# Kernel optimization log

Hardware: AMD Instinct MI355X
Metric: run time of the kernel (lower is better)

## Reference

```python
import jax, jax.numpy as jnp
from jax import lax
import numpy as np

NUM_LAYERS = 256
EPS = 1e-12


def setup_inputs() -> dict:
    key = jax.random.key(0)
    # values in [0.9, 1.1) so the 256-step multiplicative chain stays O(1)
    x = 0.9 + 0.2 * jax.random.uniform(key, (4, 19, 512, 512), dtype=jnp.float32)
    return {"x": x}


def _maxpool3x3_same(x):
    # torch MaxPool2d(kernel=3, stride=1, padding=1): pad value acts as -inf
    return lax.reduce_window(
        x, -jnp.inf, lax.max,
        window_dimensions=(1, 1, 3, 3),
        window_strides=(1, 1, 1, 1),
        padding=[(0, 0), (0, 0), (1, 1), (1, 1)],
    )


def reference(x):
    initial = x
    cur = -x
    one = jnp.float32(1.0)
    cur = cur.at[:, :, 0, :].set(one)
    cur = cur.at[:, :, -1, :].set(one)
    cur = cur.at[:, :, :, 0].set(one)
    cur = cur.at[:, :, :, -1].set(one)

    def step(c, _):
        return _maxpool3x3_same(c) * initial, None

    cur, _ = lax.scan(step, cur, None, length=NUM_LAYERS)
    # F.normalize default: L2 over dim=1, eps=1e-12
    norm = jnp.sqrt(jnp.sum(cur * cur, axis=1, keepdims=True))
    normed = cur / jnp.maximum(norm, EPS)
    return normed * initial
```

## Files before the change

### kernel.cpp

```cpp
#include <hip/hip_runtime.h>
#include <math.h>

#define BB 4
#define CC 19
#define HH 512
#define WW 512
#define NSLICE (BB * CC)
#define SLICE  (HH * WW)
#define W4     (WW / 4)
#define EPS    1e-12f
#define NEGINF (-INFINITY)

#define TSTEPS 16
#define RROWS  64
#define AROWS  96
#define NPASS  16
#define RBLK   8

#define TX   64
#define TY   8
#define COLS 8
#define ROWS 12
#define THREADS 512

struct F8 { float4 a, b; };

__device__ __forceinline__ float dpp_up(float src) {
    int o = __builtin_amdgcn_update_dpp(__float_as_int(NEGINF), __float_as_int(src),
                                        0x138 , 0xF, 0xF, false);
    return __int_as_float(o);
}
__device__ __forceinline__ float dpp_dn(float src) {
    int o = __builtin_amdgcn_update_dpp(__float_as_int(NEGINF), __float_as_int(src),
                                        0x130 , 0xF, 0xF, false);
    return __int_as_float(o);
}

__global__ void init_kernel(const float* __restrict__ x, float* __restrict__ cur) {
    int t = blockIdx.x * blockDim.x + threadIdx.x;
    const float4* x4 = (const float4*)x;
    float4* c4 = (float4*)cur;
    float4 v = x4[t];
    int pix = t << 2;
    int s = pix & (SLICE - 1);
    int i = s >> 9;
    int j0 = s & 511;
    float4 o;
    o.x = -v.x; o.y = -v.y; o.z = -v.z; o.w = -v.w;
    if (i == 0 || i == HH - 1) {
        o.x = 1.0f; o.y = 1.0f; o.z = 1.0f; o.w = 1.0f;
    } else {
        if (j0 == 0)        o.x = 1.0f;
        if (j0 == WW - 4)   o.w = 1.0f;
    }
    c4[t] = o;
}

__global__ __launch_bounds__(THREADS, 1)
void pass_kernel(const float* __restrict__ in, const float* __restrict__ xg,
                 float* __restrict__ out) {
    const int tid  = threadIdx.x;
    const int tx   = tid & 63;
    const int ty   = tid >> 6;
    const int g    = (blockIdx.x & 7) * (NSLICE * RBLK / 8) + (blockIdx.x >> 3);
    const int bc   = g / RBLK;
    const int brow = g % RBLK;
    const int gstart = brow * RROWS - TSTEPS;
    const int row0   = gstart + ty * ROWS;
    const int col0   = tx * COLS;
    const size_t sbase = (size_t)bc * SLICE;

    __shared__ float Tb[2][TY][TX * 9];
    __shared__ float Bb[2][TY][TX * 9];

    const float4 neg4 = make_float4(NEGINF, NEGINF, NEGINF, NEGINF);
    const float4 one4 = make_float4(1.f, 1.f, 1.f, 1.f);

    float4 cl[ROWS], cr[ROWS], xl[ROWS], xr_[ROWS];

#pragma unroll
    for (int r = 0; r < ROWS; ++r) {
        int grow = row0 + r;
        if (grow >= 0 && grow < HH) {
            const float4* p = (const float4*)(in + sbase + (size_t)grow * WW + col0);
            cl[r] = p[0]; cr[r] = p[1];
            const float4* q = (const float4*)(xg + sbase + (size_t)grow * WW + col0);
            xl[r] = q[0]; xr_[r] = q[1];
        } else {
            cl[r] = neg4; cr[r] = neg4; xl[r] = one4; xr_[r] = one4;
        }
    }

    auto hrow = [&](float4 a, float4 b) -> F8 {
        float lpx = dpp_up(b.w);
        float rpx = dpp_dn(a.x);
        F8 h;
        h.a.x = fmaxf(fmaxf(lpx, a.x), a.y);
        h.a.y = fmaxf(fmaxf(a.x, a.y), a.z);
        h.a.z = fmaxf(fmaxf(a.y, a.z), a.w);
        h.a.w = fmaxf(fmaxf(a.z, a.w), b.x);
        h.b.x = fmaxf(fmaxf(a.w, b.x), b.y);
        h.b.y = fmaxf(fmaxf(b.x, b.y), b.z);
        h.b.z = fmaxf(fmaxf(b.y, b.z), b.w);
        h.b.w = fmaxf(fmaxf(b.z, b.w), rpx);
        return h;
    };

    for (int t = 0; t < TSTEPS; ++t) {
        const int buf = t & 1;
        float* tp = &Tb[buf][ty][tx * 9];
        float* bp = &Bb[buf][ty][tx * 9];
        tp[0] = cl[0].x;  tp[1] = cl[0].y;  tp[2] = cl[0].z;  tp[3] = cl[0].w;
        tp[4] = cr[0].x;  tp[5] = cr[0].y;  tp[6] = cr[0].z;  tp[7] = cr[0].w;
        bp[0] = cl[11].x; bp[1] = cl[11].y; bp[2] = cl[11].z; bp[3] = cl[11].w;
        bp[4] = cr[11].x; bp[5] = cr[11].y; bp[6] = cr[11].z; bp[7] = cr[11].w;
        __syncthreads();

        float4 upA, upB, dnA, dnB;
        if (ty > 0) {
            const float* q = &Bb[buf][ty - 1][tx * 9];
            upA = make_float4(q[0], q[1], q[2], q[3]);
            upB = make_float4(q[4], q[5], q[6], q[7]);
        } else { upA = neg4; upB = neg4; }
        if (ty < TY - 1) {
            const float* q = &Tb[buf][ty + 1][tx * 9];
            dnA = make_float4(q[0], q[1], q[2], q[3]);
            dnB = make_float4(q[4], q[5], q[6], q[7]);
        } else { dnA = neg4; dnB = neg4; }

        F8 hA = hrow(upA, upB);
        F8 hB = hrow(cl[0], cr[0]);
#pragma unroll
        for (int r = 0; r < ROWS; ++r) {
            F8 hC;
            if (r + 1 < ROWS) hC = hrow(cl[r + 1], cr[r + 1]);
            else              hC = hrow(dnA, dnB);
            float4 vl, vr;
            vl.x = fmaxf(fmaxf(hA.a.x, hB.a.x), hC.a.x);
            vl.y = fmaxf(fmaxf(hA.a.y, hB.a.y), hC.a.y);
            vl.z = fmaxf(fmaxf(hA.a.z, hB.a.z), hC.a.z);
            vl.w = fmaxf(fmaxf(hA.a.w, hB.a.w), hC.a.w);
            vr.x = fmaxf(fmaxf(hA.b.x, hB.b.x), hC.b.x);
            vr.y = fmaxf(fmaxf(hA.b.y, hB.b.y), hC.b.y);
            vr.z = fmaxf(fmaxf(hA.b.z, hB.b.z), hC.b.z);
            vr.w = fmaxf(fmaxf(hA.b.w, hB.b.w), hC.b.w);
            cl[r].x = vl.x * xl[r].x;  cl[r].y = vl.y * xl[r].y;
            cl[r].z = vl.z * xl[r].z;  cl[r].w = vl.w * xl[r].w;
            cr[r].x = vr.x * xr_[r].x; cr[r].y = vr.y * xr_[r].y;
            cr[r].z = vr.z * xr_[r].z; cr[r].w = vr.w * xr_[r].w;
            hA = hB; hB = hC;
        }
#pragma unroll
        for (int r = 0; r < ROWS; ++r) {
            int grow = row0 + r;
            if (grow < 0 || grow >= HH) { cl[r] = neg4; cr[r] = neg4; }
        }
    }

#pragma unroll
    for (int r = 0; r < ROWS; ++r) {
        int a = ty * ROWS + r;
        if (a >= TSTEPS && a < TSTEPS + RROWS) {
            int grow = row0 + r;
            float4* p = (float4*)(out + sbase + (size_t)grow * WW + col0);
            p[0] = cl[r]; p[1] = cr[r];
        }
    }
}

__global__ void norm_kernel(const float* __restrict__ cur,
                            const float* __restrict__ x,
                            float* __restrict__ out) {
    int t = blockIdx.x * blockDim.x + threadIdx.x;
    int j4 = t & (W4 - 1);
    int i  = (t >> 7) & (HH - 1);
    int b  = t >> 16;
    size_t off = (size_t)b * CC * SLICE + (size_t)i * WW + (j4 << 2);

    float4 vals[CC];
    float sx = 0.f, sy = 0.f, sz = 0.f, sw = 0.f;
#pragma unroll
    for (int c = 0; c < CC; ++c) {
        float4 v = *(const float4*)(cur + off + (size_t)c * SLICE);
        vals[c] = v;
        sx += v.x * v.x; sy += v.y * v.y; sz += v.z * v.z; sw += v.w * v.w;
    }
    float4 r;
    r.x = 1.0f / fmaxf(sqrtf(sx), EPS);
    r.y = 1.0f / fmaxf(sqrtf(sy), EPS);
    r.z = 1.0f / fmaxf(sqrtf(sz), EPS);
    r.w = 1.0f / fmaxf(sqrtf(sw), EPS);
#pragma unroll
    for (int c = 0; c < CC; ++c) {
        float4 xv = *(const float4*)(x + off + (size_t)c * SLICE);
        float4 o;
        o.x = vals[c].x * xv.x * r.x;
        o.y = vals[c].y * xv.y * r.y;
        o.z = vals[c].z * xv.z * r.z;
        o.w = vals[c].w * xv.w * r.w;
        *(float4*)(out + off + (size_t)c * SLICE) = o;
    }
}

extern "C" void kernel_launch(void* const* d_in, const int* in_sizes, int n_in,
                              void* d_out, int out_size, void* d_ws, size_t ws_size,
                              hipStream_t stream) {
    const float* x = (const float*)d_in[0];
    float* out = (float*)d_out;
    float* ws  = (float*)d_ws;

    const int initBlocks = NSLICE * SLICE / 4 / 256;
    const int passBlocks = NSLICE * RBLK;
    const int normBlocks = BB * HH * W4 / 256;

    init_kernel<<<initBlocks, 256, 0, stream>>>(x, ws);
    float* a = ws;
    float* b = out;
    for (int it = 0; it < NPASS; ++it) {
        pass_kernel<<<passBlocks, THREADS, 0, stream>>>(a, x, b);
        float* tmp = a; a = b; b = tmp;
    }
    norm_kernel<<<normBlocks, 256, 0, stream>>>(ws, x, out);
}
```

Baseline: 2.218 ms.

## Split pass grid into big and small row tiles to balance the tail wave

The pass kernel body becomes a template over rows per thread and output rows per block. The grid is remapped so 512 blocks process 64-row tiles with 12 rows per thread, covering 28 slices fully and the first 384 rows of the rest. Another 192 blocks process the remaining rows as 32-row tiles with 8 rows per thread. The aim is to shrink the partial final wave over the CUs, at the cost of more halo recomputation per output row in the small tiles.

```diff
diff --git a/kernel.cpp b/kernel.cpp
--- a/kernel.cpp
+++ b/kernel.cpp
@@ -12,15 +12,14 @@
 #define NEGINF (-INFINITY)
 
 #define TSTEPS 16
-#define RROWS  64
-#define AROWS  96
 #define NPASS  16
-#define RBLK   8
+
+#define NBIG   512
+#define NSMALL 192
 
 #define TX   64
 #define TY   8
 #define COLS 8
-#define ROWS 12
 #define THREADS 512
 
 struct F8 { float4 a, b; };
@@ -56,30 +55,28 @@
     c4[t] = o;
 }
 
-__global__ __launch_bounds__(THREADS, 1)
-void pass_kernel(const float* __restrict__ in, const float* __restrict__ xg,
-                 float* __restrict__ out) {
+template<int R, int RR>
+__device__ __forceinline__ void pass_body(const float* __restrict__ in,
+                                          const float* __restrict__ xg,
+                                          float* __restrict__ out,
+                                          int bc, int tr0,
+                                          float (&Tb)[2][TY][TX * 9],
+                                          float (&Bb)[2][TY][TX * 9]) {
     const int tid  = threadIdx.x;
     const int tx   = tid & 63;
     const int ty   = tid >> 6;
-    const int g    = (blockIdx.x & 7) * (NSLICE * RBLK / 8) + (blockIdx.x >> 3);
-    const int bc   = g / RBLK;
-    const int brow = g % RBLK;
-    const int gstart = brow * RROWS - TSTEPS;
-    const int row0   = gstart + ty * ROWS;
+    const int gstart = tr0 - TSTEPS;
+    const int row0   = gstart + ty * R;
     const int col0   = tx * COLS;
     const size_t sbase = (size_t)bc * SLICE;
 
-    __shared__ float Tb[2][TY][TX * 9];
-    __shared__ float Bb[2][TY][TX * 9];
-
     const float4 neg4 = make_float4(NEGINF, NEGINF, NEGINF, NEGINF);
     const float4 one4 = make_float4(1.f, 1.f, 1.f, 1.f);
 
-    float4 cl[ROWS], cr[ROWS], xl[ROWS], xr_[ROWS];
-
-#pragma unroll
-    for (int r = 0; r < ROWS; ++r) {
+    float4 cl[R], cr[R], xl[R], xr_[R];
+
+#pragma unroll
+    for (int r = 0; r < R; ++r) {
         int grow = row0 + r;
         if (grow >= 0 && grow < HH) {
             const float4* p = (const float4*)(in + sbase + (size_t)grow * WW + col0);
@@ -110,10 +107,10 @@
         const int buf = t & 1;
         float* tp = &Tb[buf][ty][tx * 9];
         float* bp = &Bb[buf][ty][tx * 9];
-        tp[0] = cl[0].x;  tp[1] = cl[0].y;  tp[2] = cl[0].z;  tp[3] = cl[0].w;
-        tp[4] = cr[0].x;  tp[5] = cr[0].y;  tp[6] = cr[0].z;  tp[7] = cr[0].w;
-        bp[0] = cl[11].x; bp[1] = cl[11].y; bp[2] = cl[11].z; bp[3] = cl[11].w;
-        bp[4] = cr[11].x; bp[5] = cr[11].y; bp[6] = cr[11].z; bp[7] = cr[11].w;
+        tp[0] = cl[0].x;      tp[1] = cl[0].y;      tp[2] = cl[0].z;      tp[3] = cl[0].w;
+        tp[4] = cr[0].x;      tp[5] = cr[0].y;      tp[6] = cr[0].z;      tp[7] = cr[0].w;
+        bp[0] = cl[R - 1].x;  bp[1] = cl[R - 1].y;  bp[2] = cl[R - 1].z;  bp[3] = cl[R - 1].w;
+        bp[4] = cr[R - 1].x;  bp[5] = cr[R - 1].y;  bp[6] = cr[R - 1].z;  bp[7] = cr[R - 1].w;
         __syncthreads();
 
         float4 upA, upB, dnA, dnB;
@@ -131,10 +128,10 @@
         F8 hA = hrow(upA, upB);
         F8 hB = hrow(cl[0], cr[0]);
 #pragma unroll
-        for (int r = 0; r < ROWS; ++r) {
+        for (int r = 0; r < R; ++r) {
             F8 hC;
-            if (r + 1 < ROWS) hC = hrow(cl[r + 1], cr[r + 1]);
-            else              hC = hrow(dnA, dnB);
+            if (r + 1 < R) hC = hrow(cl[r + 1], cr[r + 1]);
+            else           hC = hrow(dnA, dnB);
             float4 vl, vr;
             vl.x = fmaxf(fmaxf(hA.a.x, hB.a.x), hC.a.x);
             vl.y = fmaxf(fmaxf(hA.a.y, hB.a.y), hC.a.y);
@@ -151,20 +148,48 @@
             hA = hB; hB = hC;
         }
 #pragma unroll
-        for (int r = 0; r < ROWS; ++r) {
+        for (int r = 0; r < R; ++r) {
             int grow = row0 + r;
             if (grow < 0 || grow >= HH) { cl[r] = neg4; cr[r] = neg4; }
         }
     }
 
 #pragma unroll
-    for (int r = 0; r < ROWS; ++r) {
-        int a = ty * ROWS + r;
-        if (a >= TSTEPS && a < TSTEPS + RROWS) {
+    for (int r = 0; r < R; ++r) {
+        int a = ty * R + r;
+        if (a >= TSTEPS && a < TSTEPS + RR) {
             int grow = row0 + r;
             float4* p = (float4*)(out + sbase + (size_t)grow * WW + col0);
             p[0] = cl[r]; p[1] = cr[r];
         }
+    }
+}
+
+__global__ __launch_bounds__(THREADS, 1)
+void pass_kernel(const float* __restrict__ in, const float* __restrict__ xg,
+                 float* __restrict__ out) {
+    __shared__ float Tb[2][TY][TX * 9];
+    __shared__ float Bb[2][TY][TX * 9];
+
+    const int bid = blockIdx.x;
+    if (bid < NBIG) {
+        const int g = (bid & 7) * (NBIG / 8) + (bid >> 3);
+        int bc, tr0;
+        if (g < 28 * 8) {
+            bc  = g >> 3;
+            tr0 = (g & 7) << 6;
+        } else {
+            int g2 = g - 28 * 8;
+            bc  = 28 + g2 / 6;
+            tr0 = (g2 % 6) << 6;
+        }
+        pass_body<12, 64>(in, xg, out, bc, tr0, Tb, Bb);
+    } else {
+        const int sb = bid - NBIG;
+        const int h  = (sb & 7) * (NSMALL / 8) + (sb >> 3);
+        const int bc  = 28 + (h >> 2);
+        const int tr0 = 384 + ((h & 3) << 5);
+        pass_body<8, 32>(in, xg, out, bc, tr0, Tb, Bb);
     }
 }
 
@@ -210,7 +235,7 @@
     float* ws  = (float*)d_ws;
 
     const int initBlocks = NSLICE * SLICE / 4 / 256;
-    const int passBlocks = NSLICE * RBLK;
+    const int passBlocks = NBIG + NSMALL;
     const int normBlocks = BB * HH * W4 / 256;
 
     init_kernel<<<initBlocks, 256, 0, stream>>>(x, ws);
```

After: 2.074 ms. -6.5%, faster.
